# Kernel optimization log

Hardware: AMD Instinct MI355X
Metric: run time of the kernel (lower is better)

Reference implementation:

```python
import jax, jax.numpy as jnp
import numpy as np

NSIDE = 128
NPIX = 12 * NSIDE * NSIDE          # HEALPix pixel count, nested ordering
WIN = 16                           # window = 4x4 nested child block (w=1)
SHIFT = WIN // 2
EPS = 1e-5


def _ln(x, g, b):
    mu = x.mean(-1, keepdims=True)
    var = ((x - mu) ** 2).mean(-1, keepdims=True)
    return (x - mu) * jax.lax.rsqrt(var + EPS) * g + b


def _window_attn(x, wq, bq, wp, bp, n_heads):
    B, N, C = x.shape
    D = C // n_heads
    nw = N // WIN
    qkv = (x @ wq + bq).reshape(B, nw, WIN, 3, n_heads, D)
    q, k, v = jnp.moveaxis(qkv, 3, 0)
    q = jnp.swapaxes(q, 2, 3)
    k = jnp.swapaxes(k, 2, 3)
    v = jnp.swapaxes(v, 2, 3)
    scores = jnp.einsum('bwhqd,bwhkd->bwhqk', q, k) * (D ** -0.5)
    attn = jax.nn.softmax(scores, axis=-1)
    out = jnp.einsum('bwhqk,bwhkd->bwhqd', attn, v)
    out = jnp.swapaxes(out, 2, 3).reshape(B, N, C)
    return out @ wp + bp


def _transformer_block(x, p, shift, n_heads):
    if shift:
        x = jnp.roll(x, -SHIFT, axis=1)          # cyclic shift along nested index
    x = x + _window_attn(_ln(x, p['ln1_g'], p['ln1_b']),
                         p['w_qkv'], p['b_qkv'], p['w_proj'], p['b_proj'], n_heads)
    h = _ln(x, p['ln2_g'], p['ln2_b'])
    x = x + jax.nn.gelu(h @ p['w_mlp1'] + p['b_mlp1'], approximate=False) @ p['w_mlp2'] + p['b_mlp2']
    if shift:
        x = jnp.roll(x, SHIFT, axis=1)
    return x


def _forward(x, w_ff1, b_ff1, ln1_g, ln1_b, w_qkv, b_qkv, w_proj, b_proj,
             ln2_g, ln2_b, w_mlp1, b_mlp1, w_mlp2, b_mlp2, w_ff2, b_ff2,
             n_heads=4):
    residual = x
    h = jax.nn.gelu(x @ w_ff1 + b_ff1, approximate=False)
    for i, shift in enumerate((False, True)):
        p = dict(ln1_g=ln1_g[i], ln1_b=ln1_b[i], w_qkv=w_qkv[i], b_qkv=b_qkv[i],
                 w_proj=w_proj[i], b_proj=b_proj[i], ln2_g=ln2_g[i], ln2_b=ln2_b[i],
                 w_mlp1=w_mlp1[i], b_mlp1=b_mlp1[i], w_mlp2=w_mlp2[i], b_mlp2=b_mlp2[i])
        h = _transformer_block(h, p, shift, n_heads)
    return residual + h @ w_ff2 + b_ff2


def setup_inputs() -> dict:
    key = jax.random.key(0)
    ks = jax.random.split(key, 8)
    F, C, M = 64, 128, 512  # node_feat_dim, node_hidden_dim, mlp hidden
    s = 0.02
    return {
        'x': jax.random.normal(ks[0], (1, NPIX, F), jnp.float32),
        'w_ff1': jax.random.normal(ks[1], (F, C), jnp.float32) * s,
        'b_ff1': jnp.zeros((C,), jnp.float32),
        'ln1_g': jnp.ones((2, C), jnp.float32),
        'ln1_b': jnp.zeros((2, C), jnp.float32),
        'w_qkv': jax.random.normal(ks[2], (2, C, 3 * C), jnp.float32) * s,
        'b_qkv': jnp.zeros((2, 3 * C), jnp.float32),
        'w_proj': jax.random.normal(ks[3], (2, C, C), jnp.float32) * s,
        'b_proj': jnp.zeros((2, C), jnp.float32),
        'ln2_g': jnp.ones((2, C), jnp.float32),
        'ln2_b': jnp.zeros((2, C), jnp.float32),
        'w_mlp1': jax.random.normal(ks[4], (2, C, M), jnp.float32) * s,
        'b_mlp1': jnp.zeros((2, M), jnp.float32),
        'w_mlp2': jax.random.normal(ks[5], (2, M, C), jnp.float32) * s,
        'b_mlp2': jnp.zeros((2, C), jnp.float32),
        'w_ff2': jax.random.normal(ks[6], (C, F), jnp.float32) * s,
        'b_ff2': jnp.zeros((F,), jnp.float32),
    }


def reference(x, w_ff1, b_ff1, ln1_g, ln1_b, w_qkv, b_qkv, w_proj, b_proj,
              ln2_g, ln2_b, w_mlp1, b_mlp1, w_mlp2, b_mlp2, w_ff2, b_ff2):
    return _forward(x, w_ff1, b_ff1, ln1_g, ln1_b, w_qkv, b_qkv, w_proj, b_proj,
                    ln2_g, ln2_b, w_mlp1, b_mlp1, w_mlp2, b_mlp2, w_ff2, b_ff2)
```

## Files before the change

### kernel.cpp

```cpp
#include <hip/hip_runtime.h>
#include <hip/hip_bf16.h>
#include <math.h>

#define NPIX 196608
#define SCALE_Q 0.17677669529663687f

typedef __attribute__((ext_vector_type(4))) float f32x4;
typedef __attribute__((ext_vector_type(8))) short short8;
typedef __attribute__((ext_vector_type(4))) short short4v;
typedef __hip_bfloat16 bf16;

__device__ __forceinline__ float gelu_f(float x) {
    float yy = 1.5957691216057308f * (x + 0.044715f * x * x * x);
    float e = __expf(yy);
    return x - x * __builtin_amdgcn_rcpf(e + 1.0f);
}

__device__ __forceinline__ short bfbits(float f) {
    bf16 h = __float2bfloat16(f);
    return *reinterpret_cast<short*>(&h);
}

__device__ __forceinline__ short8 ldsA(const bf16* buf, int row, int el) {
    return *reinterpret_cast<const short8*>(buf + row * 128 + (el ^ ((row & 7) << 3)));
}
__device__ __forceinline__ short8 ldsA64(const bf16* buf, int row, int el) {
    return *reinterpret_cast<const short8*>(buf + row * 64 + (el ^ ((row & 7) << 3)));
}
__device__ __forceinline__ short8 gld8(const bf16* p) {
    return *reinterpret_cast<const short8*>(p);
}

__global__ __launch_bounds__(256) void k_convert(
    const float* __restrict__ wff1, const float* __restrict__ wqkv,
    const float* __restrict__ wproj, const float* __restrict__ wmlp1,
    const float* __restrict__ wmlp2, const float* __restrict__ wff2,
    bf16* __restrict__ dst)
{
    int gid = blockIdx.x * 256 + threadIdx.x;
    if (gid < 8192) {
        int n = gid >> 6, k = gid & 63;
        dst[gid] = __float2bfloat16(wff1[k * 128 + n]);
    } else if (gid < 106496) {
        int r = gid - 8192; int l = r / 49152; r -= l * 49152;
        int n = r >> 7, k = r & 127;
        dst[gid] = __float2bfloat16(wqkv[l * 49152 + k * 384 + n]);
    } else if (gid < 139264) {
        int r = gid - 106496; int l = r / 16384; r -= l * 16384;
        int n = r >> 7, k = r & 127;
        dst[gid] = __float2bfloat16(wproj[l * 16384 + k * 128 + n]);
    } else if (gid < 270336) {
        int r = gid - 139264; int l = r >> 16; r &= 65535;
        int n = r >> 7, k = r & 127;
        dst[gid] = __float2bfloat16(wmlp1[l * 65536 + k * 512 + n]);
    } else if (gid < 401408) {
        int r = gid - 270336; int l = r >> 16; r &= 65535;
        int n = r >> 9, k = r & 511;
        dst[gid] = __float2bfloat16(wmlp2[l * 65536 + k * 128 + n]);
    } else if (gid < 409600) {
        int r = gid - 401408;
        int n = r >> 7, k = r & 127;
        dst[gid] = __float2bfloat16(wff2[k * 64 + n]);
    }
}

template <int OFFSET, int MODE>
__global__ __launch_bounds__(256, 3) void k_block(
    const float* __restrict__ x, float* __restrict__ h,
    const bf16* __restrict__ wf1t, const float* __restrict__ bf1,
    const float* __restrict__ g1, const float* __restrict__ be1,
    const bf16* __restrict__ wqt, const float* __restrict__ bq,
    const bf16* __restrict__ wpt, const float* __restrict__ bp,
    const float* __restrict__ g2, const float* __restrict__ be2,
    const bf16* __restrict__ w1t, const float* __restrict__ b1,
    const bf16* __restrict__ w2t, const float* __restrict__ b2,
    const bf16* __restrict__ wf2t, const float* __restrict__ bf2,
    float* __restrict__ out)
{
    __shared__ __align__(16) bf16 bufA[8192];
    __shared__ __align__(16) bf16 bufB[8192];
    __shared__ __align__(16) bf16 bufC[8192];
    const int tid = threadIdx.x, base = blockIdx.x * 64;
    const int wid = tid >> 6, lrow = tid & 15, lgrp = (tid >> 4) & 3;
    const int cb0 = wid * 32;

    f32x4 hraw[2][4];

    if (MODE == 0) {
        short8 wf1[2][2];
#pragma unroll
        for (int nt = 0; nt < 2; ++nt)
#pragma unroll
            for (int kk = 0; kk < 2; ++kk)
                wf1[nt][kk] = gld8(wf1t + (size_t)(cb0 + nt * 16 + lrow) * 64 + kk * 32 + lgrp * 8);
        {
            int row = tid >> 2, q = tid & 3;
#pragma unroll
            for (int s = 0; s < 2; ++s) {
                int gg = q + s * 4;
                const float4* src = reinterpret_cast<const float4*>(x + (size_t)(base + row) * 64 + gg * 8);
                float4 v0 = src[0], v1 = src[1];
                short8 w;
                w[0] = bfbits(v0.x); w[1] = bfbits(v0.y); w[2] = bfbits(v0.z); w[3] = bfbits(v0.w);
                w[4] = bfbits(v1.x); w[5] = bfbits(v1.y); w[6] = bfbits(v1.z); w[7] = bfbits(v1.w);
                *reinterpret_cast<short8*>(&bufC[row * 64 + ((gg * 8) ^ ((row & 7) << 3))]) = w;
            }
        }
        __syncthreads();
        short8 xb1[4][2];
#pragma unroll
        for (int tt = 0; tt < 4; ++tt)
#pragma unroll
            for (int kk = 0; kk < 2; ++kk)
                xb1[tt][kk] = ldsA64(bufC, tt * 16 + lrow, kk * 32 + lgrp * 8);
        __syncthreads();
#pragma unroll
        for (int nt = 0; nt < 2; ++nt) {
            float4 bv = *reinterpret_cast<const float4*>(bf1 + cb0 + nt * 16 + lgrp * 4);
#pragma unroll
            for (int tt = 0; tt < 4; ++tt) {
                f32x4 d = {0.f, 0.f, 0.f, 0.f};
#pragma unroll
                for (int kk = 0; kk < 2; ++kk)
                    d = __builtin_amdgcn_mfma_f32_16x16x32_bf16(wf1[nt][kk], xb1[tt][kk], d, 0, 0, 0);
                f32x4 r;
                r[0] = gelu_f(d[0] + bv.x); r[1] = gelu_f(d[1] + bv.y);
                r[2] = gelu_f(d[2] + bv.z); r[3] = gelu_f(d[3] + bv.w);
                hraw[nt][tt] = r;
            }
        }
    } else {
#pragma unroll
        for (int nt = 0; nt < 2; ++nt)
#pragma unroll
            for (int tt = 0; tt < 4; ++tt) {
                int tok = base + OFFSET + tt * 16 + lrow; if (tok >= NPIX) tok -= NPIX;
                float4 hv = *reinterpret_cast<const float4*>(h + (size_t)tok * 128 + cb0 + nt * 16 + lgrp * 4);
                f32x4 r; r[0] = hv.x; r[1] = hv.y; r[2] = hv.z; r[3] = hv.w;
                hraw[nt][tt] = r;
            }
        __syncthreads();
    }

    float2* ws = reinterpret_cast<float2*>(bufC);
#pragma unroll
    for (int tt = 0; tt < 4; ++tt) {
        float s = 0.f, q = 0.f;
#pragma unroll
        for (int nt = 0; nt < 2; ++nt)
#pragma unroll
            for (int i = 0; i < 4; ++i) { float v = hraw[nt][tt][i]; s += v; q += v * v; }
        s += __shfl_xor(s, 16, 64); s += __shfl_xor(s, 32, 64);
        q += __shfl_xor(q, 16, 64); q += __shfl_xor(q, 32, 64);
        if (lgrp == 0) { float2 t2; t2.x = s; t2.y = q; ws[wid * 64 + tt * 16 + lrow] = t2; }
    }
    __syncthreads();
    {
        float mu[4], rstd[4];
#pragma unroll
        for (int tt = 0; tt < 4; ++tt) {
            float s = 0.f, q = 0.f;
#pragma unroll
            for (int w = 0; w < 4; ++w) {
                float2 t2 = ws[w * 64 + tt * 16 + lrow];
                s += t2.x; q += t2.y;
            }
            float m = s * (1.f / 128.f);
            mu[tt] = m;
            rstd[tt] = rsqrtf(q * (1.f / 128.f) - m * m + 1e-5f);
        }
        float4 gv[2], bev[2];
#pragma unroll
        for (int nt = 0; nt < 2; ++nt) {
            gv[nt]  = *reinterpret_cast<const float4*>(g1 + cb0 + nt * 16 + lgrp * 4);
            bev[nt] = *reinterpret_cast<const float4*>(be1 + cb0 + nt * 16 + lgrp * 4);
        }
#pragma unroll
        for (int nt = 0; nt < 2; ++nt)
#pragma unroll
            for (int tt = 0; tt < 4; ++tt) {
                short4v pk;
                pk[0] = bfbits((hraw[nt][tt][0] - mu[tt]) * rstd[tt] * gv[nt].x + bev[nt].x);
                pk[1] = bfbits((hraw[nt][tt][1] - mu[tt]) * rstd[tt] * gv[nt].y + bev[nt].y);
                pk[2] = bfbits((hraw[nt][tt][2] - mu[tt]) * rstd[tt] * gv[nt].z + bev[nt].z);
                pk[3] = bfbits((hraw[nt][tt][3] - mu[tt]) * rstd[tt] * gv[nt].w + bev[nt].w);
                int row = tt * 16 + lrow;
                int c = cb0 + nt * 16 + lgrp * 4;
                *reinterpret_cast<short4v*>(&bufA[row * 128 + (c ^ ((row & 7) << 3))]) = pk;
            }
    }

    const int qc = wid * 96;
    short8 wq0[2][4], wq1[2][4];
#pragma unroll
    for (int j = 0; j < 2; ++j)
#pragma unroll
        for (int kk = 0; kk < 4; ++kk)
            wq0[j][kk] = gld8(wqt + (size_t)(qc + j * 16 + lrow) * 128 + kk * 32 + lgrp * 8);
    __syncthreads();

    short8 xb[4][4];
#pragma unroll
    for (int tt = 0; tt < 4; ++tt)
#pragma unroll
        for (int kk = 0; kk < 4; ++kk)
            xb[tt][kk] = ldsA(bufA, tt * 16 + lrow, kk * 32 + lgrp * 8);
    __syncthreads();

#define QKV_TILE(WF, NB)                                                            \
    {                                                                               \
        const int cb = qc + (NB) * 16;                                              \
        float4 bqv = *reinterpret_cast<const float4*>(bq + cb + lgrp * 4);          \
        _Pragma("unroll")                                                           \
        for (int tt = 0; tt < 4; ++tt) {                                            \
            f32x4 d = {0.f, 0.f, 0.f, 0.f};                                         \
            _Pragma("unroll")                                                       \
            for (int kk = 0; kk < 4; ++kk)                                          \
                d = __builtin_amdgcn_mfma_f32_16x16x32_bf16(WF[kk], xb[tt][kk], d, 0, 0, 0); \
            int row = tt * 16 + lrow;                                               \
            if (cb < 128) {                                                         \
                int c = cb + lgrp * 4;                                              \
                short4v pk;                                                         \
                pk[0] = bfbits((d[0] + bqv.x) * SCALE_Q); pk[1] = bfbits((d[1] + bqv.y) * SCALE_Q); \
                pk[2] = bfbits((d[2] + bqv.z) * SCALE_Q); pk[3] = bfbits((d[3] + bqv.w) * SCALE_Q); \
                *reinterpret_cast<short4v*>(&bufA[row * 128 + (c ^ ((row & 7) << 3))]) = pk; \
            } else if (cb < 256) {                                                  \
                int c = cb - 128 + lgrp * 4;                                        \
                short4v pk;                                                         \
                pk[0] = bfbits(d[0] + bqv.x); pk[1] = bfbits(d[1] + bqv.y);         \
                pk[2] = bfbits(d[2] + bqv.z); pk[3] = bfbits(d[3] + bqv.w);         \
                *reinterpret_cast<short4v*>(&bufB[row * 128 + (c ^ ((row & 7) << 3))]) = pk; \
            } else {                                                                \
                int db = cb - 256 + lgrp * 4;                                       \
                bufC[tt * 2048 + (db + 0) * 16 + lrow] = __float2bfloat16(d[0] + bqv.x); \
                bufC[tt * 2048 + (db + 1) * 16 + lrow] = __float2bfloat16(d[1] + bqv.y); \
                bufC[tt * 2048 + (db + 2) * 16 + lrow] = __float2bfloat16(d[2] + bqv.z); \
                bufC[tt * 2048 + (db + 3) * 16 + lrow] = __float2bfloat16(d[3] + bqv.w); \
            }                                                                       \
        }                                                                           \
    }

#pragma unroll
    for (int j = 0; j < 2; ++j)
#pragma unroll
        for (int kk = 0; kk < 4; ++kk)
            wq1[j][kk] = gld8(wqt + (size_t)(qc + (j + 2) * 16 + lrow) * 128 + kk * 32 + lgrp * 8);
    QKV_TILE(wq0[0], 0) QKV_TILE(wq0[1], 1)
#pragma unroll
    for (int j = 0; j < 2; ++j)
#pragma unroll
        for (int kk = 0; kk < 4; ++kk)
            wq0[j][kk] = gld8(wqt + (size_t)(qc + (j + 4) * 16 + lrow) * 128 + kk * 32 + lgrp * 8);
    QKV_TILE(wq1[0], 2) QKV_TILE(wq1[1], 3)
    QKV_TILE(wq0[0], 4) QKV_TILE(wq0[1], 5)
    __syncthreads();

    short8 wfp[2][4];
#pragma unroll
    for (int nt = 0; nt < 2; ++nt)
#pragma unroll
        for (int kk = 0; kk < 4; ++kk)
            wfp[nt][kk] = gld8(wpt + (size_t)(cb0 + nt * 16 + lrow) * 128 + kk * 32 + lgrp * 8);

    float p[4][4];
#pragma unroll
    for (int hh = 0; hh < 4; ++hh) {
        short8 aq = ldsA(bufA, wid * 16 + lrow, hh * 32 + lgrp * 8);
        short8 bk = ldsA(bufB, wid * 16 + lrow, hh * 32 + lgrp * 8);
        f32x4 z = {0.f, 0.f, 0.f, 0.f};
        f32x4 s = __builtin_amdgcn_mfma_f32_16x16x32_bf16(aq, bk, z, 0, 0, 0);
#pragma unroll
        for (int i = 0; i < 4; ++i) {
            float m_ = s[i];
            m_ = fmaxf(m_, __shfl_xor(m_, 1, 64));
            m_ = fmaxf(m_, __shfl_xor(m_, 2, 64));
            m_ = fmaxf(m_, __shfl_xor(m_, 4, 64));
            m_ = fmaxf(m_, __shfl_xor(m_, 8, 64));
            float e = __expf(s[i] - m_);
            float sum = e;
            sum += __shfl_xor(sum, 1, 64);
            sum += __shfl_xor(sum, 2, 64);
            sum += __shfl_xor(sum, 4, 64);
            sum += __shfl_xor(sum, 8, 64);
            p[hh][i] = e * __builtin_amdgcn_rcpf(sum);
        }
    }
    bf16* pl = bufB + wid * 2048;
#pragma unroll
    for (int hh = 0; hh < 4; ++hh)
#pragma unroll
        for (int i = 0; i < 4; ++i)
            pl[hh * 256 + (lgrp * 4 + i) * 16 + lrow] = __float2bfloat16(p[hh][i]);

    short8 z8 = {0, 0, 0, 0, 0, 0, 0, 0};
#pragma unroll
    for (int dt = 0; dt < 8; ++dt) {
        int hh = dt >> 1;
        short8 av = z8, bv = z8;
        if (lgrp < 2) {
            av = *reinterpret_cast<const short8*>(&bufC[wid * 2048 + (dt * 16 + lrow) * 16 + lgrp * 8]);
            bv = *reinterpret_cast<const short8*>(&pl[hh * 256 + lrow * 16 + lgrp * 8]);
        }
        f32x4 z = {0.f, 0.f, 0.f, 0.f};
        f32x4 o = __builtin_amdgcn_mfma_f32_16x16x32_bf16(av, bv, z, 0, 0, 0);
        int row = wid * 16 + lrow;
        int c = dt * 16 + lgrp * 4;
        short4v pk;
        pk[0] = bfbits(o[0]); pk[1] = bfbits(o[1]); pk[2] = bfbits(o[2]); pk[3] = bfbits(o[3]);
        *reinterpret_cast<short4v*>(&bufA[row * 128 + (c ^ ((row & 7) << 3))]) = pk;
    }
    __syncthreads();

    short8 af[4][4];
#pragma unroll
    for (int tt = 0; tt < 4; ++tt)
#pragma unroll
        for (int kk = 0; kk < 4; ++kk)
            af[tt][kk] = ldsA(bufA, tt * 16 + lrow, kk * 32 + lgrp * 8);
    f32x4 hres[2][4];
#pragma unroll
    for (int nt = 0; nt < 2; ++nt) {
        float4 bpv = *reinterpret_cast<const float4*>(bp + cb0 + nt * 16 + lgrp * 4);
#pragma unroll
        for (int tt = 0; tt < 4; ++tt) {
            f32x4 d = {0.f, 0.f, 0.f, 0.f};
#pragma unroll
            for (int kk = 0; kk < 4; ++kk)
                d = __builtin_amdgcn_mfma_f32_16x16x32_bf16(wfp[nt][kk], af[tt][kk], d, 0, 0, 0);
            f32x4 r = hraw[nt][tt];
            r[0] += bpv.x + d[0]; r[1] += bpv.y + d[1];
            r[2] += bpv.z + d[2]; r[3] += bpv.w + d[3];
            hres[nt][tt] = r;
        }
    }

#pragma unroll
    for (int tt = 0; tt < 4; ++tt) {
        float s = 0.f, q = 0.f;
#pragma unroll
        for (int nt = 0; nt < 2; ++nt)
#pragma unroll
            for (int i = 0; i < 4; ++i) { float v = hres[nt][tt][i]; s += v; q += v * v; }
        s += __shfl_xor(s, 16, 64); s += __shfl_xor(s, 32, 64);
        q += __shfl_xor(q, 16, 64); q += __shfl_xor(q, 32, 64);
        if (lgrp == 0) { float2 t2; t2.x = s; t2.y = q; ws[wid * 64 + tt * 16 + lrow] = t2; }
    }
    __syncthreads();
    short8 w1f[2][2][4];
    {
        float mu[4], rstd[4];
#pragma unroll
        for (int tt = 0; tt < 4; ++tt) {
            float s = 0.f, q = 0.f;
#pragma unroll
            for (int w = 0; w < 4; ++w) {
                float2 t2 = ws[w * 64 + tt * 16 + lrow];
                s += t2.x; q += t2.y;
            }
            float m = s * (1.f / 128.f);
            mu[tt] = m;
            rstd[tt] = rsqrtf(q * (1.f / 128.f) - m * m + 1e-5f);
        }
        float4 gv[2], bev[2];
#pragma unroll
        for (int nt = 0; nt < 2; ++nt) {
            gv[nt]  = *reinterpret_cast<const float4*>(g2 + cb0 + nt * 16 + lgrp * 4);
            bev[nt] = *reinterpret_cast<const float4*>(be2 + cb0 + nt * 16 + lgrp * 4);
        }
#pragma unroll
        for (int nt = 0; nt < 2; ++nt)
#pragma unroll
            for (int tt = 0; tt < 4; ++tt) {
                short4v pk;
                pk[0] = bfbits((hres[nt][tt][0] - mu[tt]) * rstd[tt] * gv[nt].x + bev[nt].x);
                pk[1] = bfbits((hres[nt][tt][1] - mu[tt]) * rstd[tt] * gv[nt].y + bev[nt].y);
                pk[2] = bfbits((hres[nt][tt][2] - mu[tt]) * rstd[tt] * gv[nt].z + bev[nt].z);
                pk[3] = bfbits((hres[nt][tt][3] - mu[tt]) * rstd[tt] * gv[nt].w + bev[nt].w);
                int row = tt * 16 + lrow;
                int c = cb0 + nt * 16 + lgrp * 4;
                *reinterpret_cast<short4v*>(&bufB[row * 128 + (c ^ ((row & 7) << 3))]) = pk;
            }
    }
#pragma unroll
    for (int nt = 0; nt < 2; ++nt)
#pragma unroll
        for (int kk = 0; kk < 4; ++kk)
            w1f[0][nt][kk] = gld8(w1t + (size_t)(cb0 + nt * 16 + lrow) * 128 + kk * 32 + lgrp * 8);
    __syncthreads();

    f32x4 acc2[2][4];
#pragma unroll
    for (int nt = 0; nt < 2; ++nt)
#pragma unroll
        for (int tt = 0; tt < 4; ++tt) acc2[nt][tt] = (f32x4){0.f, 0.f, 0.f, 0.f};

#pragma unroll
    for (int ch = 0; ch < 4; ++ch) {
        short8 w2f[2][4];
#pragma unroll
        for (int nt = 0; nt < 2; ++nt)
#pragma unroll
            for (int kk = 0; kk < 4; ++kk)
                w2f[nt][kk] = gld8(w2t + (size_t)(cb0 + nt * 16 + lrow) * 512 + ch * 128 + kk * 32 + lgrp * 8);
        float4 b1v[2];
#pragma unroll
        for (int nt = 0; nt < 2; ++nt)
            b1v[nt] = *reinterpret_cast<const float4*>(b1 + ch * 128 + cb0 + nt * 16 + lgrp * 4);
#pragma unroll
        for (int tt = 0; tt < 4; ++tt) {
            short8 xf[4];
#pragma unroll
            for (int kk = 0; kk < 4; ++kk)
                xf[kk] = ldsA(bufB, tt * 16 + lrow, kk * 32 + lgrp * 8);
#pragma unroll
            for (int nt = 0; nt < 2; ++nt) {
                f32x4 d = {0.f, 0.f, 0.f, 0.f};
#pragma unroll
                for (int kk = 0; kk < 4; ++kk)
                    d = __builtin_amdgcn_mfma_f32_16x16x32_bf16(w1f[ch & 1][nt][kk], xf[kk], d, 0, 0, 0);
                short4v pk;
                pk[0] = bfbits(gelu_f(d[0] + b1v[nt].x)); pk[1] = bfbits(gelu_f(d[1] + b1v[nt].y));
                pk[2] = bfbits(gelu_f(d[2] + b1v[nt].z)); pk[3] = bfbits(gelu_f(d[3] + b1v[nt].w));
                int row = tt * 16 + lrow;
                int c = cb0 + nt * 16 + lgrp * 4;
                *reinterpret_cast<short4v*>(&bufA[row * 128 + (c ^ ((row & 7) << 3))]) = pk;
            }
        }
        __syncthreads();
        if (ch < 3) {
#pragma unroll
            for (int nt = 0; nt < 2; ++nt)
#pragma unroll
                for (int kk = 0; kk < 4; ++kk)
                    w1f[(ch + 1) & 1][nt][kk] =
                        gld8(w1t + (size_t)((ch + 1) * 128 + cb0 + nt * 16 + lrow) * 128 + kk * 32 + lgrp * 8);
        }
#pragma unroll
        for (int tt = 0; tt < 4; ++tt) {
            short8 uf[4];
#pragma unroll
            for (int kk = 0; kk < 4; ++kk)
                uf[kk] = ldsA(bufA, tt * 16 + lrow, kk * 32 + lgrp * 8);
#pragma unroll
            for (int nt = 0; nt < 2; ++nt)
#pragma unroll
                for (int kk = 0; kk < 4; ++kk)
                    acc2[nt][tt] = __builtin_amdgcn_mfma_f32_16x16x32_bf16(
                        w2f[nt][kk], uf[kk], acc2[nt][tt], 0, 0, 0);
        }
        __syncthreads();
    }

    if (MODE == 0) {
#pragma unroll
        for (int nt = 0; nt < 2; ++nt) {
            const int n0 = cb0 + nt * 16 + lgrp * 4;
            float4 b2v = *reinterpret_cast<const float4*>(b2 + n0);
#pragma unroll
            for (int tt = 0; tt < 4; ++tt) {
                int tok = base + OFFSET + tt * 16 + lrow; if (tok >= NPIX) tok -= NPIX;
                float4 ov;
                ov.x = hres[nt][tt][0] + b2v.x + acc2[nt][tt][0];
                ov.y = hres[nt][tt][1] + b2v.y + acc2[nt][tt][1];
                ov.z = hres[nt][tt][2] + b2v.z + acc2[nt][tt][2];
                ov.w = hres[nt][tt][3] + b2v.w + acc2[nt][tt][3];
                *reinterpret_cast<float4*>(h + (size_t)tok * 128 + n0) = ov;
            }
        }
    } else {
        short8 wff[4];
#pragma unroll
        for (int kk = 0; kk < 4; ++kk)
            wff[kk] = gld8(wf2t + (size_t)(wid * 16 + lrow) * 128 + kk * 32 + lgrp * 8);
        float4 xv[4];
#pragma unroll
        for (int tt = 0; tt < 4; ++tt) {
            int tok = base + OFFSET + tt * 16 + lrow; if (tok >= NPIX) tok -= NPIX;
            xv[tt] = *reinterpret_cast<const float4*>(x + (size_t)tok * 64 + wid * 16 + lgrp * 4);
        }
#pragma unroll
        for (int nt = 0; nt < 2; ++nt) {
            const int n0 = cb0 + nt * 16 + lgrp * 4;
            float4 b2v = *reinterpret_cast<const float4*>(b2 + n0);
#pragma unroll
            for (int tt = 0; tt < 4; ++tt) {
                short4v pk;
                pk[0] = bfbits(hres[nt][tt][0] + b2v.x + acc2[nt][tt][0]);
                pk[1] = bfbits(hres[nt][tt][1] + b2v.y + acc2[nt][tt][1]);
                pk[2] = bfbits(hres[nt][tt][2] + b2v.z + acc2[nt][tt][2]);
                pk[3] = bfbits(hres[nt][tt][3] + b2v.w + acc2[nt][tt][3]);
                int row = tt * 16 + lrow;
                int c = cb0 + nt * 16 + lgrp * 4;
                *reinterpret_cast<short4v*>(&bufB[row * 128 + (c ^ ((row & 7) << 3))]) = pk;
            }
        }
        __syncthreads();
        float4 bfv = *reinterpret_cast<const float4*>(bf2 + wid * 16 + lgrp * 4);
#pragma unroll
        for (int tt = 0; tt < 4; ++tt) {
            short8 bfr[4];
#pragma unroll
            for (int kk = 0; kk < 4; ++kk)
                bfr[kk] = ldsA(bufB, tt * 16 + lrow, kk * 32 + lgrp * 8);
            f32x4 d = {0.f, 0.f, 0.f, 0.f};
#pragma unroll
            for (int kk = 0; kk < 4; ++kk)
                d = __builtin_amdgcn_mfma_f32_16x16x32_bf16(wff[kk], bfr[kk], d, 0, 0, 0);
            int tok = base + OFFSET + tt * 16 + lrow; if (tok >= NPIX) tok -= NPIX;
            float4 ov;
            ov.x = xv[tt].x + bfv.x + d[0]; ov.y = xv[tt].y + bfv.y + d[1];
            ov.z = xv[tt].z + bfv.z + d[2]; ov.w = xv[tt].w + bfv.w + d[3];
            *reinterpret_cast<float4*>(out + (size_t)tok * 64 + wid * 16 + lgrp * 4) = ov;
        }
    }
#undef QKV_TILE
}

extern "C" void kernel_launch(void* const* d_in, const int* in_sizes, int n_in,
                              void* d_out, int out_size, void* d_ws, size_t ws_size,
                              hipStream_t stream) {
    (void)in_sizes; (void)n_in; (void)out_size; (void)ws_size;
    const float* x      = (const float*)d_in[0];
    const float* w_ff1  = (const float*)d_in[1];
    const float* b_ff1  = (const float*)d_in[2];
    const float* ln1_g  = (const float*)d_in[3];
    const float* ln1_b  = (const float*)d_in[4];
    const float* w_qkv  = (const float*)d_in[5];
    const float* b_qkv  = (const float*)d_in[6];
    const float* w_proj = (const float*)d_in[7];
    const float* b_proj = (const float*)d_in[8];
    const float* ln2_g  = (const float*)d_in[9];
    const float* ln2_b  = (const float*)d_in[10];
    const float* w_mlp1 = (const float*)d_in[11];
    const float* b_mlp1 = (const float*)d_in[12];
    const float* w_mlp2 = (const float*)d_in[13];
    const float* b_mlp2 = (const float*)d_in[14];
    const float* w_ff2  = (const float*)d_in[15];
    const float* b_ff2  = (const float*)d_in[16];
    float* out = (float*)d_out;

    float* h = (float*)d_ws;
    bf16* wbf = (bf16*)((char*)d_ws + (size_t)NPIX * 128 * 4);
    bf16* ff1t  = wbf;
    bf16* qkvt  = wbf + 8192;
    bf16* projt = wbf + 106496;
    bf16* mlp1t = wbf + 139264;
    bf16* mlp2t = wbf + 270336;
    bf16* ff2t  = wbf + 401408;

    dim3 blk(256);
    k_convert<<<1600, blk, 0, stream>>>(w_ff1, w_qkv, w_proj, w_mlp1, w_mlp2, w_ff2, wbf);

    const int NB = NPIX / 64;
    k_block<0, 0><<<NB, blk, 0, stream>>>(x, h,
        ff1t, b_ff1,
        ln1_g, ln1_b, qkvt, b_qkv, projt, b_proj,
        ln2_g, ln2_b, mlp1t, b_mlp1, mlp2t, b_mlp2,
        ff2t, b_ff2, out);

    k_block<8, 1><<<NB, blk, 0, stream>>>(x, h,
        ff1t, b_ff1,
        ln1_g + 128, ln1_b + 128, qkvt + 49152, b_qkv + 384, projt + 16384, b_proj + 128,
        ln2_g + 128, ln2_b + 128, mlp1t + 65536, b_mlp1 + 512, mlp2t + 65536, b_mlp2 + 128,
        ff2t, b_ff2, out);
}
```

Baseline: 488.0 us.

## Restructure block kernel to one wavefront per 16-token window without barriers

Each workgroup now holds a single 64-lane wavefront that owns one 16-token window and computes all 128 output channels itself. The old design had 256 threads handling 64 tokens with channels split across four waves. Because one wave now does everything, the __syncthreads barriers and the cross-wave LayerNorm reduction through shared memory disappear, and LDS per block shrinks to 16 KB. In exchange, every wave streams the full weight matrices from global/L2 memory, with no sharing across waves and no prefetch double-buffering, so weight traffic per token rises roughly fourfold. It also uses 4x more blocks.

```diff
diff --git a/kernel.cpp b/kernel.cpp
--- a/kernel.cpp
+++ b/kernel.cpp
@@ -21,12 +21,6 @@
     return *reinterpret_cast<short*>(&h);
 }
 
-__device__ __forceinline__ short8 ldsA(const bf16* buf, int row, int el) {
-    return *reinterpret_cast<const short8*>(buf + row * 128 + (el ^ ((row & 7) << 3)));
-}
-__device__ __forceinline__ short8 ldsA64(const bf16* buf, int row, int el) {
-    return *reinterpret_cast<const short8*>(buf + row * 64 + (el ^ ((row & 7) << 3)));
-}
 __device__ __forceinline__ short8 gld8(const bf16* p) {
     return *reinterpret_cast<const short8*>(p);
 }
@@ -65,7 +59,7 @@
 }
 
 template <int OFFSET, int MODE>
-__global__ __launch_bounds__(256, 3) void k_block(
+__global__ __launch_bounds__(64, 2) void k_block(
     const float* __restrict__ x, float* __restrict__ h,
     const bf16* __restrict__ wf1t, const float* __restrict__ bf1,
     const float* __restrict__ g1, const float* __restrict__ be1,
@@ -77,196 +71,139 @@
     const bf16* __restrict__ wf2t, const float* __restrict__ bf2,
     float* __restrict__ out)
 {
-    __shared__ __align__(16) bf16 bufA[8192];
-    __shared__ __align__(16) bf16 bufB[8192];
-    __shared__ __align__(16) bf16 bufC[8192];
-    const int tid = threadIdx.x, base = blockIdx.x * 64;
-    const int wid = tid >> 6, lrow = tid & 15, lgrp = (tid >> 4) & 3;
-    const int cb0 = wid * 32;
-
-    f32x4 hraw[2][4];
+    __shared__ __align__(16) bf16 S[8192];
+    bf16* XN1 = S;
+    bf16* QQ  = S + 2048;
+    bf16* KK  = S + 4096;
+    bf16* VT  = S + 6144;
+    const int lane = threadIdx.x;
+    const int lrow = lane & 15, lgrp = lane >> 4;
+    const int base = blockIdx.x * 16;
+    int tok = base + OFFSET + lrow; if (tok >= NPIX) tok -= NPIX;
+    const int sw = (lrow & 7) << 3;
+
+    f32x4 hraw[8];
 
     if (MODE == 0) {
-        short8 wf1[2][2];
-#pragma unroll
-        for (int nt = 0; nt < 2; ++nt)
+        const float4* src = reinterpret_cast<const float4*>(x + (size_t)(base + lrow) * 64 + lgrp * 16);
+        float4 v0 = src[0], v1 = src[1], v2 = src[2], v3 = src[3];
+        short8 w0, w1;
+        w0[0]=bfbits(v0.x); w0[1]=bfbits(v0.y); w0[2]=bfbits(v0.z); w0[3]=bfbits(v0.w);
+        w0[4]=bfbits(v1.x); w0[5]=bfbits(v1.y); w0[6]=bfbits(v1.z); w0[7]=bfbits(v1.w);
+        w1[0]=bfbits(v2.x); w1[1]=bfbits(v2.y); w1[2]=bfbits(v2.z); w1[3]=bfbits(v2.w);
+        w1[4]=bfbits(v3.x); w1[5]=bfbits(v3.y); w1[6]=bfbits(v3.z); w1[7]=bfbits(v3.w);
+        *reinterpret_cast<short8*>(&KK[lrow * 64 + ((lgrp * 16) ^ sw)]) = w0;
+        *reinterpret_cast<short8*>(&KK[lrow * 64 + ((lgrp * 16 + 8) ^ sw)]) = w1;
+        short8 xb1[2];
+#pragma unroll
+        for (int kk = 0; kk < 2; ++kk)
+            xb1[kk] = *reinterpret_cast<const short8*>(&KK[lrow * 64 + ((kk * 32 + lgrp * 8) ^ sw)]);
+#pragma unroll
+        for (int nt = 0; nt < 8; ++nt) {
+            short8 wf[2];
 #pragma unroll
             for (int kk = 0; kk < 2; ++kk)
-                wf1[nt][kk] = gld8(wf1t + (size_t)(cb0 + nt * 16 + lrow) * 64 + kk * 32 + lgrp * 8);
-        {
-            int row = tid >> 2, q = tid & 3;
-#pragma unroll
-            for (int s = 0; s < 2; ++s) {
-                int gg = q + s * 4;
-                const float4* src = reinterpret_cast<const float4*>(x + (size_t)(base + row) * 64 + gg * 8);
-                float4 v0 = src[0], v1 = src[1];
-                short8 w;
-                w[0] = bfbits(v0.x); w[1] = bfbits(v0.y); w[2] = bfbits(v0.z); w[3] = bfbits(v0.w);
-                w[4] = bfbits(v1.x); w[5] = bfbits(v1.y); w[6] = bfbits(v1.z); w[7] = bfbits(v1.w);
-                *reinterpret_cast<short8*>(&bufC[row * 64 + ((gg * 8) ^ ((row & 7) << 3))]) = w;
-            }
-        }
-        __syncthreads();
-        short8 xb1[4][2];
-#pragma unroll
-        for (int tt = 0; tt < 4; ++tt)
+                wf[kk] = gld8(wf1t + (size_t)(nt * 16 + lrow) * 64 + kk * 32 + lgrp * 8);
+            f32x4 d = {0.f, 0.f, 0.f, 0.f};
 #pragma unroll
             for (int kk = 0; kk < 2; ++kk)
-                xb1[tt][kk] = ldsA64(bufC, tt * 16 + lrow, kk * 32 + lgrp * 8);
-        __syncthreads();
-#pragma unroll
-        for (int nt = 0; nt < 2; ++nt) {
-            float4 bv = *reinterpret_cast<const float4*>(bf1 + cb0 + nt * 16 + lgrp * 4);
-#pragma unroll
-            for (int tt = 0; tt < 4; ++tt) {
-                f32x4 d = {0.f, 0.f, 0.f, 0.f};
-#pragma unroll
-                for (int kk = 0; kk < 2; ++kk)
-                    d = __builtin_amdgcn_mfma_f32_16x16x32_bf16(wf1[nt][kk], xb1[tt][kk], d, 0, 0, 0);
-                f32x4 r;
-                r[0] = gelu_f(d[0] + bv.x); r[1] = gelu_f(d[1] + bv.y);
-                r[2] = gelu_f(d[2] + bv.z); r[3] = gelu_f(d[3] + bv.w);
-                hraw[nt][tt] = r;
-            }
+                d = __builtin_amdgcn_mfma_f32_16x16x32_bf16(wf[kk], xb1[kk], d, 0, 0, 0);
+            float4 bv = *reinterpret_cast<const float4*>(bf1 + nt * 16 + lgrp * 4);
+            f32x4 r;
+            r[0] = gelu_f(d[0] + bv.x); r[1] = gelu_f(d[1] + bv.y);
+            r[2] = gelu_f(d[2] + bv.z); r[3] = gelu_f(d[3] + bv.w);
+            hraw[nt] = r;
         }
     } else {
 #pragma unroll
-        for (int nt = 0; nt < 2; ++nt)
-#pragma unroll
-            for (int tt = 0; tt < 4; ++tt) {
-                int tok = base + OFFSET + tt * 16 + lrow; if (tok >= NPIX) tok -= NPIX;
-                float4 hv = *reinterpret_cast<const float4*>(h + (size_t)tok * 128 + cb0 + nt * 16 + lgrp * 4);
-                f32x4 r; r[0] = hv.x; r[1] = hv.y; r[2] = hv.z; r[3] = hv.w;
-                hraw[nt][tt] = r;
-            }
-        __syncthreads();
-    }
-
-    float2* ws = reinterpret_cast<float2*>(bufC);
-#pragma unroll
-    for (int tt = 0; tt < 4; ++tt) {
+        for (int nt = 0; nt < 8; ++nt) {
+            float4 hv = *reinterpret_cast<const float4*>(h + (size_t)tok * 128 + nt * 16 + lgrp * 4);
+            f32x4 r; r[0] = hv.x; r[1] = hv.y; r[2] = hv.z; r[3] = hv.w;
+            hraw[nt] = r;
+        }
+    }
+
+    {
         float s = 0.f, q = 0.f;
 #pragma unroll
-        for (int nt = 0; nt < 2; ++nt)
-#pragma unroll
-            for (int i = 0; i < 4; ++i) { float v = hraw[nt][tt][i]; s += v; q += v * v; }
+        for (int nt = 0; nt < 8; ++nt)
+#pragma unroll
+            for (int i = 0; i < 4; ++i) { float v = hraw[nt][i]; s += v; q += v * v; }
         s += __shfl_xor(s, 16, 64); s += __shfl_xor(s, 32, 64);
         q += __shfl_xor(q, 16, 64); q += __shfl_xor(q, 32, 64);
-        if (lgrp == 0) { float2 t2; t2.x = s; t2.y = q; ws[wid * 64 + tt * 16 + lrow] = t2; }
-    }
-    __syncthreads();
-    {
-        float mu[4], rstd[4];
-#pragma unroll
-        for (int tt = 0; tt < 4; ++tt) {
-            float s = 0.f, q = 0.f;
-#pragma unroll
-            for (int w = 0; w < 4; ++w) {
-                float2 t2 = ws[w * 64 + tt * 16 + lrow];
-                s += t2.x; q += t2.y;
-            }
-            float m = s * (1.f / 128.f);
-            mu[tt] = m;
-            rstd[tt] = rsqrtf(q * (1.f / 128.f) - m * m + 1e-5f);
-        }
-        float4 gv[2], bev[2];
-#pragma unroll
-        for (int nt = 0; nt < 2; ++nt) {
-            gv[nt]  = *reinterpret_cast<const float4*>(g1 + cb0 + nt * 16 + lgrp * 4);
-            bev[nt] = *reinterpret_cast<const float4*>(be1 + cb0 + nt * 16 + lgrp * 4);
-        }
-#pragma unroll
-        for (int nt = 0; nt < 2; ++nt)
-#pragma unroll
-            for (int tt = 0; tt < 4; ++tt) {
-                short4v pk;
-                pk[0] = bfbits((hraw[nt][tt][0] - mu[tt]) * rstd[tt] * gv[nt].x + bev[nt].x);
-                pk[1] = bfbits((hraw[nt][tt][1] - mu[tt]) * rstd[tt] * gv[nt].y + bev[nt].y);
-                pk[2] = bfbits((hraw[nt][tt][2] - mu[tt]) * rstd[tt] * gv[nt].z + bev[nt].z);
-                pk[3] = bfbits((hraw[nt][tt][3] - mu[tt]) * rstd[tt] * gv[nt].w + bev[nt].w);
-                int row = tt * 16 + lrow;
-                int c = cb0 + nt * 16 + lgrp * 4;
-                *reinterpret_cast<short4v*>(&bufA[row * 128 + (c ^ ((row & 7) << 3))]) = pk;
-            }
-    }
-
-    const int qc = wid * 96;
-    short8 wq0[2][4], wq1[2][4];
-#pragma unroll
-    for (int j = 0; j < 2; ++j)
-#pragma unroll
-        for (int kk = 0; kk < 4; ++kk)
-            wq0[j][kk] = gld8(wqt + (size_t)(qc + j * 16 + lrow) * 128 + kk * 32 + lgrp * 8);
-    __syncthreads();
-
-    short8 xb[4][4];
-#pragma unroll
-    for (int tt = 0; tt < 4; ++tt)
-#pragma unroll
-        for (int kk = 0; kk < 4; ++kk)
-            xb[tt][kk] = ldsA(bufA, tt * 16 + lrow, kk * 32 + lgrp * 8);
-    __syncthreads();
-
-#define QKV_TILE(WF, NB)                                                            \
-    {                                                                               \
-        const int cb = qc + (NB) * 16;                                              \
-        float4 bqv = *reinterpret_cast<const float4*>(bq + cb + lgrp * 4);          \
-        _Pragma("unroll")                                                           \
-        for (int tt = 0; tt < 4; ++tt) {                                            \
-            f32x4 d = {0.f, 0.f, 0.f, 0.f};                                         \
-            _Pragma("unroll")                                                       \
-            for (int kk = 0; kk < 4; ++kk)                                          \
-                d = __builtin_amdgcn_mfma_f32_16x16x32_bf16(WF[kk], xb[tt][kk], d, 0, 0, 0); \
-            int row = tt * 16 + lrow;                                               \
-            if (cb < 128) {                                                         \
-                int c = cb + lgrp * 4;                                              \
-                short4v pk;                                                         \
-                pk[0] = bfbits((d[0] + bqv.x) * SCALE_Q); pk[1] = bfbits((d[1] + bqv.y) * SCALE_Q); \
-                pk[2] = bfbits((d[2] + bqv.z) * SCALE_Q); pk[3] = bfbits((d[3] + bqv.w) * SCALE_Q); \
-                *reinterpret_cast<short4v*>(&bufA[row * 128 + (c ^ ((row & 7) << 3))]) = pk; \
-            } else if (cb < 256) {                                                  \
-                int c = cb - 128 + lgrp * 4;                                        \
-                short4v pk;                                                         \
-                pk[0] = bfbits(d[0] + bqv.x); pk[1] = bfbits(d[1] + bqv.y);         \
-                pk[2] = bfbits(d[2] + bqv.z); pk[3] = bfbits(d[3] + bqv.w);         \
-                *reinterpret_cast<short4v*>(&bufB[row * 128 + (c ^ ((row & 7) << 3))]) = pk; \
-            } else {                                                                \
-                int db = cb - 256 + lgrp * 4;                                       \
-                bufC[tt * 2048 + (db + 0) * 16 + lrow] = __float2bfloat16(d[0] + bqv.x); \
-                bufC[tt * 2048 + (db + 1) * 16 + lrow] = __float2bfloat16(d[1] + bqv.y); \
-                bufC[tt * 2048 + (db + 2) * 16 + lrow] = __float2bfloat16(d[2] + bqv.z); \
-                bufC[tt * 2048 + (db + 3) * 16 + lrow] = __float2bfloat16(d[3] + bqv.w); \
-            }                                                                       \
-        }                                                                           \
-    }
-
-#pragma unroll
-    for (int j = 0; j < 2; ++j)
-#pragma unroll
-        for (int kk = 0; kk < 4; ++kk)
-            wq1[j][kk] = gld8(wqt + (size_t)(qc + (j + 2) * 16 + lrow) * 128 + kk * 32 + lgrp * 8);
-    QKV_TILE(wq0[0], 0) QKV_TILE(wq0[1], 1)
-#pragma unroll
-    for (int j = 0; j < 2; ++j)
-#pragma unroll
-        for (int kk = 0; kk < 4; ++kk)
-            wq0[j][kk] = gld8(wqt + (size_t)(qc + (j + 4) * 16 + lrow) * 128 + kk * 32 + lgrp * 8);
-    QKV_TILE(wq1[0], 2) QKV_TILE(wq1[1], 3)
-    QKV_TILE(wq0[0], 4) QKV_TILE(wq0[1], 5)
-    __syncthreads();
-
-    short8 wfp[2][4];
-#pragma unroll
-    for (int nt = 0; nt < 2; ++nt)
-#pragma unroll
-        for (int kk = 0; kk < 4; ++kk)
-            wfp[nt][kk] = gld8(wpt + (size_t)(cb0 + nt * 16 + lrow) * 128 + kk * 32 + lgrp * 8);
+        float mu = s * (1.f / 128.f);
+        float rstd = rsqrtf(q * (1.f / 128.f) - mu * mu + 1e-5f);
+#pragma unroll
+        for (int nt = 0; nt < 8; ++nt) {
+            float4 gv  = *reinterpret_cast<const float4*>(g1 + nt * 16 + lgrp * 4);
+            float4 bev = *reinterpret_cast<const float4*>(be1 + nt * 16 + lgrp * 4);
+            short4v pk;
+            pk[0] = bfbits((hraw[nt][0] - mu) * rstd * gv.x + bev.x);
+            pk[1] = bfbits((hraw[nt][1] - mu) * rstd * gv.y + bev.y);
+            pk[2] = bfbits((hraw[nt][2] - mu) * rstd * gv.z + bev.z);
+            pk[3] = bfbits((hraw[nt][3] - mu) * rstd * gv.w + bev.w);
+            *reinterpret_cast<short4v*>(&XN1[lrow * 128 + ((nt * 16 + lgrp * 4) ^ sw)]) = pk;
+        }
+    }
+    short8 xb[4];
+#pragma unroll
+    for (int kk = 0; kk < 4; ++kk)
+        xb[kk] = *reinterpret_cast<const short8*>(&XN1[lrow * 128 + ((kk * 32 + lgrp * 8) ^ sw)]);
+
+#pragma unroll
+    for (int nt = 0; nt < 8; ++nt) {
+        short8 wf[4];
+#pragma unroll
+        for (int kk = 0; kk < 4; ++kk)
+            wf[kk] = gld8(wqt + (size_t)(nt * 16 + lrow) * 128 + kk * 32 + lgrp * 8);
+        f32x4 d = {0.f, 0.f, 0.f, 0.f};
+#pragma unroll
+        for (int kk = 0; kk < 4; ++kk)
+            d = __builtin_amdgcn_mfma_f32_16x16x32_bf16(wf[kk], xb[kk], d, 0, 0, 0);
+        float4 bv = *reinterpret_cast<const float4*>(bq + nt * 16 + lgrp * 4);
+        short4v pk;
+        pk[0] = bfbits((d[0] + bv.x) * SCALE_Q); pk[1] = bfbits((d[1] + bv.y) * SCALE_Q);
+        pk[2] = bfbits((d[2] + bv.z) * SCALE_Q); pk[3] = bfbits((d[3] + bv.w) * SCALE_Q);
+        *reinterpret_cast<short4v*>(&QQ[lrow * 128 + ((nt * 16 + lgrp * 4) ^ sw)]) = pk;
+    }
+#pragma unroll
+    for (int nt = 0; nt < 8; ++nt) {
+        short8 wf[4];
+#pragma unroll
+        for (int kk = 0; kk < 4; ++kk)
+            wf[kk] = gld8(wqt + (size_t)(128 + nt * 16 + lrow) * 128 + kk * 32 + lgrp * 8);
+        f32x4 d = {0.f, 0.f, 0.f, 0.f};
+#pragma unroll
+        for (int kk = 0; kk < 4; ++kk)
+            d = __builtin_amdgcn_mfma_f32_16x16x32_bf16(wf[kk], xb[kk], d, 0, 0, 0);
+        float4 bv = *reinterpret_cast<const float4*>(bq + 128 + nt * 16 + lgrp * 4);
+        short4v pk;
+        pk[0] = bfbits(d[0] + bv.x); pk[1] = bfbits(d[1] + bv.y);
+        pk[2] = bfbits(d[2] + bv.z); pk[3] = bfbits(d[3] + bv.w);
+        *reinterpret_cast<short4v*>(&KK[lrow * 128 + ((nt * 16 + lgrp * 4) ^ sw)]) = pk;
+    }
+#pragma unroll
+    for (int dt = 0; dt < 8; ++dt) {
+        short8 wv[4];
+#pragma unroll
+        for (int kk = 0; kk < 4; ++kk)
+            wv[kk] = gld8(wqt + (size_t)(256 + dt * 16 + lrow) * 128 + kk * 32 + lgrp * 8);
+        f32x4 d = {0.f, 0.f, 0.f, 0.f};
+#pragma unroll
+        for (int kk = 0; kk < 4; ++kk)
+            d = __builtin_amdgcn_mfma_f32_16x16x32_bf16(xb[kk], wv[kk], d, 0, 0, 0);
+        float bv = bq[256 + dt * 16 + lrow];
+        short4v pk;
+        pk[0] = bfbits(d[0] + bv); pk[1] = bfbits(d[1] + bv);
+        pk[2] = bfbits(d[2] + bv); pk[3] = bfbits(d[3] + bv);
+        *reinterpret_cast<short4v*>(&VT[(dt * 16 + lrow) * 16 + lgrp * 4]) = pk;
+    }
 
     float p[4][4];
 #pragma unroll
     for (int hh = 0; hh < 4; ++hh) {
-        short8 aq = ldsA(bufA, wid * 16 + lrow, hh * 32 + lgrp * 8);
-        short8 bk = ldsA(bufB, wid * 16 + lrow, hh * 32 + lgrp * 8);
+        short8 aq = *reinterpret_cast<const short8*>(&QQ[lrow * 128 + ((hh * 32 + lgrp * 8) ^ sw)]);
+        short8 bk = *reinterpret_cast<const short8*>(&KK[lrow * 128 + ((hh * 32 + lgrp * 8) ^ sw)]);
         f32x4 z = {0.f, 0.f, 0.f, 0.f};
         f32x4 s = __builtin_amdgcn_mfma_f32_16x16x32_bf16(aq, bk, z, 0, 0, 0);
 #pragma unroll
@@ -285,12 +222,11 @@
             p[hh][i] = e * __builtin_amdgcn_rcpf(sum);
         }
     }
-    bf16* pl = bufB + wid * 2048;
 #pragma unroll
     for (int hh = 0; hh < 4; ++hh)
 #pragma unroll
         for (int i = 0; i < 4; ++i)
-            pl[hh * 256 + (lgrp * 4 + i) * 16 + lrow] = __float2bfloat16(p[hh][i]);
+            QQ[hh * 256 + (lgrp * 4 + i) * 16 + lrow] = __float2bfloat16(p[hh][i]);
 
     short8 z8 = {0, 0, 0, 0, 0, 0, 0, 0};
 #pragma unroll
@@ -298,222 +234,148 @@
         int hh = dt >> 1;
         short8 av = z8, bv = z8;
         if (lgrp < 2) {
-            av = *reinterpret_cast<const short8*>(&bufC[wid * 2048 + (dt * 16 + lrow) * 16 + lgrp * 8]);
-            bv = *reinterpret_cast<const short8*>(&pl[hh * 256 + lrow * 16 + lgrp * 8]);
+            av = *reinterpret_cast<const short8*>(&VT[(dt * 16 + lrow) * 16 + lgrp * 8]);
+            bv = *reinterpret_cast<const short8*>(&QQ[hh * 256 + lrow * 16 + lgrp * 8]);
         }
         f32x4 z = {0.f, 0.f, 0.f, 0.f};
         f32x4 o = __builtin_amdgcn_mfma_f32_16x16x32_bf16(av, bv, z, 0, 0, 0);
-        int row = wid * 16 + lrow;
-        int c = dt * 16 + lgrp * 4;
         short4v pk;
         pk[0] = bfbits(o[0]); pk[1] = bfbits(o[1]); pk[2] = bfbits(o[2]); pk[3] = bfbits(o[3]);
-        *reinterpret_cast<short4v*>(&bufA[row * 128 + (c ^ ((row & 7) << 3))]) = pk;
-    }
-    __syncthreads();
-
-    short8 af[4][4];
-#pragma unroll
-    for (int tt = 0; tt < 4; ++tt)
-#pragma unroll
-        for (int kk = 0; kk < 4; ++kk)
-            af[tt][kk] = ldsA(bufA, tt * 16 + lrow, kk * 32 + lgrp * 8);
-    f32x4 hres[2][4];
-#pragma unroll
-    for (int nt = 0; nt < 2; ++nt) {
-        float4 bpv = *reinterpret_cast<const float4*>(bp + cb0 + nt * 16 + lgrp * 4);
-#pragma unroll
-        for (int tt = 0; tt < 4; ++tt) {
-            f32x4 d = {0.f, 0.f, 0.f, 0.f};
-#pragma unroll
-            for (int kk = 0; kk < 4; ++kk)
-                d = __builtin_amdgcn_mfma_f32_16x16x32_bf16(wfp[nt][kk], af[tt][kk], d, 0, 0, 0);
-            f32x4 r = hraw[nt][tt];
-            r[0] += bpv.x + d[0]; r[1] += bpv.y + d[1];
-            r[2] += bpv.z + d[2]; r[3] += bpv.w + d[3];
-            hres[nt][tt] = r;
-        }
-    }
-
-#pragma unroll
-    for (int tt = 0; tt < 4; ++tt) {
+        *reinterpret_cast<short4v*>(&XN1[lrow * 128 + ((dt * 16 + lgrp * 4) ^ sw)]) = pk;
+    }
+
+    short8 af[4];
+#pragma unroll
+    for (int kk = 0; kk < 4; ++kk)
+        af[kk] = *reinterpret_cast<const short8*>(&XN1[lrow * 128 + ((kk * 32 + lgrp * 8) ^ sw)]);
+    f32x4 hres[8];
+#pragma unroll
+    for (int nt = 0; nt < 8; ++nt) {
+        short8 wf[4];
+#pragma unroll
+        for (int kk = 0; kk < 4; ++kk)
+            wf[kk] = gld8(wpt + (size_t)(nt * 16 + lrow) * 128 + kk * 32 + lgrp * 8);
+        f32x4 d = {0.f, 0.f, 0.f, 0.f};
+#pragma unroll
+        for (int kk = 0; kk < 4; ++kk)
+            d = __builtin_amdgcn_mfma_f32_16x16x32_bf16(wf[kk], af[kk], d, 0, 0, 0);
+        float4 bv = *reinterpret_cast<const float4*>(bp + nt * 16 + lgrp * 4);
+        f32x4 r = hraw[nt];
+        r[0] += bv.x + d[0]; r[1] += bv.y + d[1];
+        r[2] += bv.z + d[2]; r[3] += bv.w + d[3];
+        hres[nt] = r;
+    }
+
+    {
         float s = 0.f, q = 0.f;
 #pragma unroll
-        for (int nt = 0; nt < 2; ++nt)
-#pragma unroll
-            for (int i = 0; i < 4; ++i) { float v = hres[nt][tt][i]; s += v; q += v * v; }
+        for (int nt = 0; nt < 8; ++nt)
+#pragma unroll
+            for (int i = 0; i < 4; ++i) { float v = hres[nt][i]; s += v; q += v * v; }
         s += __shfl_xor(s, 16, 64); s += __shfl_xor(s, 32, 64);
         q += __shfl_xor(q, 16, 64); q += __shfl_xor(q, 32, 64);
-        if (lgrp == 0) { float2 t2; t2.x = s; t2.y = q; ws[wid * 64 + tt * 16 + lrow] = t2; }
-    }
-    __syncthreads();
-    short8 w1f[2][2][4];
-    {
-        float mu[4], rstd[4];
-#pragma unroll
-        for (int tt = 0; tt < 4; ++tt) {
-            float s = 0.f, q = 0.f;
-#pragma unroll
-            for (int w = 0; w < 4; ++w) {
-                float2 t2 = ws[w * 64 + tt * 16 + lrow];
-                s += t2.x; q += t2.y;
-            }
-            float m = s * (1.f / 128.f);
-            mu[tt] = m;
-            rstd[tt] = rsqrtf(q * (1.f / 128.f) - m * m + 1e-5f);
-        }
-        float4 gv[2], bev[2];
-#pragma unroll
-        for (int nt = 0; nt < 2; ++nt) {
-            gv[nt]  = *reinterpret_cast<const float4*>(g2 + cb0 + nt * 16 + lgrp * 4);
-            bev[nt] = *reinterpret_cast<const float4*>(be2 + cb0 + nt * 16 + lgrp * 4);
-        }
-#pragma unroll
-        for (int nt = 0; nt < 2; ++nt)
-#pragma unroll
-            for (int tt = 0; tt < 4; ++tt) {
-                short4v pk;
-                pk[0] = bfbits((hres[nt][tt][0] - mu[tt]) * rstd[tt] * gv[nt].x + bev[nt].x);
-                pk[1] = bfbits((hres[nt][tt][1] - mu[tt]) * rstd[tt] * gv[nt].y + bev[nt].y);
-                pk[2] = bfbits((hres[nt][tt][2] - mu[tt]) * rstd[tt] * gv[nt].z + bev[nt].z);
-                pk[3] = bfbits((hres[nt][tt][3] - mu[tt]) * rstd[tt] * gv[nt].w + bev[nt].w);
-                int row = tt * 16 + lrow;
-                int c = cb0 + nt * 16 + lgrp * 4;
-                *reinterpret_cast<short4v*>(&bufB[row * 128 + (c ^ ((row & 7) << 3))]) = pk;
-            }
-    }
-#pragma unroll
-    for (int nt = 0; nt < 2; ++nt)
-#pragma unroll
-        for (int kk = 0; kk < 4; ++kk)
-            w1f[0][nt][kk] = gld8(w1t + (size_t)(cb0 + nt * 16 + lrow) * 128 + kk * 32 + lgrp * 8);
-    __syncthreads();
-
-    f32x4 acc2[2][4];
-#pragma unroll
-    for (int nt = 0; nt < 2; ++nt)
-#pragma unroll
-        for (int tt = 0; tt < 4; ++tt) acc2[nt][tt] = (f32x4){0.f, 0.f, 0.f, 0.f};
-
+        float mu = s * (1.f / 128.f);
+        float rstd = rsqrtf(q * (1.f / 128.f) - mu * mu + 1e-5f);
+#pragma unroll
+        for (int nt = 0; nt < 8; ++nt) {
+            float4 gv  = *reinterpret_cast<const float4*>(g2 + nt * 16 + lgrp * 4);
+            float4 bev = *reinterpret_cast<const float4*>(be2 + nt * 16 + lgrp * 4);
+            short4v pk;
+            pk[0] = bfbits((hres[nt][0] - mu) * rstd * gv.x + bev.x);
+            pk[1] = bfbits((hres[nt][1] - mu) * rstd * gv.y + bev.y);
+            pk[2] = bfbits((hres[nt][2] - mu) * rstd * gv.z + bev.z);
+            pk[3] = bfbits((hres[nt][3] - mu) * rstd * gv.w + bev.w);
+            *reinterpret_cast<short4v*>(&QQ[lrow * 128 + ((nt * 16 + lgrp * 4) ^ sw)]) = pk;
+        }
+    }
+    short8 xb2[4];
+#pragma unroll
+    for (int kk = 0; kk < 4; ++kk)
+        xb2[kk] = *reinterpret_cast<const short8*>(&QQ[lrow * 128 + ((kk * 32 + lgrp * 8) ^ sw)]);
+
+    f32x4 acc2[8];
+#pragma unroll
+    for (int nt = 0; nt < 8; ++nt) acc2[nt] = (f32x4){0.f, 0.f, 0.f, 0.f};
 #pragma unroll
     for (int ch = 0; ch < 4; ++ch) {
-        short8 w2f[2][4];
-#pragma unroll
-        for (int nt = 0; nt < 2; ++nt)
-#pragma unroll
-            for (int kk = 0; kk < 4; ++kk)
-                w2f[nt][kk] = gld8(w2t + (size_t)(cb0 + nt * 16 + lrow) * 512 + ch * 128 + kk * 32 + lgrp * 8);
-        float4 b1v[2];
-#pragma unroll
-        for (int nt = 0; nt < 2; ++nt)
-            b1v[nt] = *reinterpret_cast<const float4*>(b1 + ch * 128 + cb0 + nt * 16 + lgrp * 4);
-#pragma unroll
-        for (int tt = 0; tt < 4; ++tt) {
-            short8 xf[4];
-#pragma unroll
-            for (int kk = 0; kk < 4; ++kk)
-                xf[kk] = ldsA(bufB, tt * 16 + lrow, kk * 32 + lgrp * 8);
-#pragma unroll
-            for (int nt = 0; nt < 2; ++nt) {
-                f32x4 d = {0.f, 0.f, 0.f, 0.f};
-#pragma unroll
-                for (int kk = 0; kk < 4; ++kk)
-                    d = __builtin_amdgcn_mfma_f32_16x16x32_bf16(w1f[ch & 1][nt][kk], xf[kk], d, 0, 0, 0);
-                short4v pk;
-                pk[0] = bfbits(gelu_f(d[0] + b1v[nt].x)); pk[1] = bfbits(gelu_f(d[1] + b1v[nt].y));
-                pk[2] = bfbits(gelu_f(d[2] + b1v[nt].z)); pk[3] = bfbits(gelu_f(d[3] + b1v[nt].w));
-                int row = tt * 16 + lrow;
-                int c = cb0 + nt * 16 + lgrp * 4;
-                *reinterpret_cast<short4v*>(&bufA[row * 128 + (c ^ ((row & 7) << 3))]) = pk;
-            }
-        }
-        __syncthreads();
-        if (ch < 3) {
-#pragma unroll
-            for (int nt = 0; nt < 2; ++nt)
-#pragma unroll
-                for (int kk = 0; kk < 4; ++kk)
-                    w1f[(ch + 1) & 1][nt][kk] =
-                        gld8(w1t + (size_t)((ch + 1) * 128 + cb0 + nt * 16 + lrow) * 128 + kk * 32 + lgrp * 8);
-        }
-#pragma unroll
-        for (int tt = 0; tt < 4; ++tt) {
-            short8 uf[4];
-#pragma unroll
-            for (int kk = 0; kk < 4; ++kk)
-                uf[kk] = ldsA(bufA, tt * 16 + lrow, kk * 32 + lgrp * 8);
-#pragma unroll
-            for (int nt = 0; nt < 2; ++nt)
-#pragma unroll
-                for (int kk = 0; kk < 4; ++kk)
-                    acc2[nt][tt] = __builtin_amdgcn_mfma_f32_16x16x32_bf16(
-                        w2f[nt][kk], uf[kk], acc2[nt][tt], 0, 0, 0);
-        }
-        __syncthreads();
+        bf16* UB = (ch & 1) ? VT : KK;
+#pragma unroll
+        for (int nt = 0; nt < 8; ++nt) {
+            short8 wf[4];
+#pragma unroll
+            for (int kk = 0; kk < 4; ++kk)
+                wf[kk] = gld8(w1t + (size_t)(ch * 128 + nt * 16 + lrow) * 128 + kk * 32 + lgrp * 8);
+            f32x4 d = {0.f, 0.f, 0.f, 0.f};
+#pragma unroll
+            for (int kk = 0; kk < 4; ++kk)
+                d = __builtin_amdgcn_mfma_f32_16x16x32_bf16(wf[kk], xb2[kk], d, 0, 0, 0);
+            float4 bv = *reinterpret_cast<const float4*>(b1 + ch * 128 + nt * 16 + lgrp * 4);
+            short4v pk;
+            pk[0] = bfbits(gelu_f(d[0] + bv.x)); pk[1] = bfbits(gelu_f(d[1] + bv.y));
+            pk[2] = bfbits(gelu_f(d[2] + bv.z)); pk[3] = bfbits(gelu_f(d[3] + bv.w));
+            *reinterpret_cast<short4v*>(&UB[lrow * 128 + ((nt * 16 + lgrp * 4) ^ sw)]) = pk;
+        }
+        short8 uf[4];
+#pragma unroll
+        for (int kk = 0; kk < 4; ++kk)
+            uf[kk] = *reinterpret_cast<const short8*>(&UB[lrow * 128 + ((kk * 32 + lgrp * 8) ^ sw)]);
+#pragma unroll
+        for (int nt = 0; nt < 8; ++nt) {
+            short8 wf[4];
+#pragma unroll
+            for (int kk = 0; kk < 4; ++kk)
+                wf[kk] = gld8(w2t + (size_t)(nt * 16 + lrow) * 512 + ch * 128 + kk * 32 + lgrp * 8);
+#pragma unroll
+            for (int kk = 0; kk < 4; ++kk)
+                acc2[nt] = __builtin_amdgcn_mfma_f32_16x16x32_bf16(wf[kk], uf[kk], acc2[nt], 0, 0, 0);
+        }
     }
 
     if (MODE == 0) {
 #pragma unroll
-        for (int nt = 0; nt < 2; ++nt) {
-            const int n0 = cb0 + nt * 16 + lgrp * 4;
-            float4 b2v = *reinterpret_cast<const float4*>(b2 + n0);
-#pragma unroll
-            for (int tt = 0; tt < 4; ++tt) {
-                int tok = base + OFFSET + tt * 16 + lrow; if (tok >= NPIX) tok -= NPIX;
-                float4 ov;
-                ov.x = hres[nt][tt][0] + b2v.x + acc2[nt][tt][0];
-                ov.y = hres[nt][tt][1] + b2v.y + acc2[nt][tt][1];
-                ov.z = hres[nt][tt][2] + b2v.z + acc2[nt][tt][2];
-                ov.w = hres[nt][tt][3] + b2v.w + acc2[nt][tt][3];
-                *reinterpret_cast<float4*>(h + (size_t)tok * 128 + n0) = ov;
-            }
+        for (int nt = 0; nt < 8; ++nt) {
+            float4 b2v = *reinterpret_cast<const float4*>(b2 + nt * 16 + lgrp * 4);
+            float4 ov;
+            ov.x = hres[nt][0] + b2v.x + acc2[nt][0];
+            ov.y = hres[nt][1] + b2v.y + acc2[nt][1];
+            ov.z = hres[nt][2] + b2v.z + acc2[nt][2];
+            ov.w = hres[nt][3] + b2v.w + acc2[nt][3];
+            *reinterpret_cast<float4*>(h + (size_t)tok * 128 + nt * 16 + lgrp * 4) = ov;
         }
     } else {
-        short8 wff[4];
-#pragma unroll
-        for (int kk = 0; kk < 4; ++kk)
-            wff[kk] = gld8(wf2t + (size_t)(wid * 16 + lrow) * 128 + kk * 32 + lgrp * 8);
-        float4 xv[4];
-#pragma unroll
-        for (int tt = 0; tt < 4; ++tt) {
-            int tok = base + OFFSET + tt * 16 + lrow; if (tok >= NPIX) tok -= NPIX;
-            xv[tt] = *reinterpret_cast<const float4*>(x + (size_t)tok * 64 + wid * 16 + lgrp * 4);
-        }
-#pragma unroll
-        for (int nt = 0; nt < 2; ++nt) {
-            const int n0 = cb0 + nt * 16 + lgrp * 4;
-            float4 b2v = *reinterpret_cast<const float4*>(b2 + n0);
-#pragma unroll
-            for (int tt = 0; tt < 4; ++tt) {
-                short4v pk;
-                pk[0] = bfbits(hres[nt][tt][0] + b2v.x + acc2[nt][tt][0]);
-                pk[1] = bfbits(hres[nt][tt][1] + b2v.y + acc2[nt][tt][1]);
-                pk[2] = bfbits(hres[nt][tt][2] + b2v.z + acc2[nt][tt][2]);
-                pk[3] = bfbits(hres[nt][tt][3] + b2v.w + acc2[nt][tt][3]);
-                int row = tt * 16 + lrow;
-                int c = cb0 + nt * 16 + lgrp * 4;
-                *reinterpret_cast<short4v*>(&bufB[row * 128 + (c ^ ((row & 7) << 3))]) = pk;
-            }
-        }
-        __syncthreads();
-        float4 bfv = *reinterpret_cast<const float4*>(bf2 + wid * 16 + lgrp * 4);
-#pragma unroll
-        for (int tt = 0; tt < 4; ++tt) {
-            short8 bfr[4];
-#pragma unroll
-            for (int kk = 0; kk < 4; ++kk)
-                bfr[kk] = ldsA(bufB, tt * 16 + lrow, kk * 32 + lgrp * 8);
+#pragma unroll
+        for (int nt = 0; nt < 8; ++nt) {
+            float4 b2v = *reinterpret_cast<const float4*>(b2 + nt * 16 + lgrp * 4);
+            short4v pk;
+            pk[0] = bfbits(hres[nt][0] + b2v.x + acc2[nt][0]);
+            pk[1] = bfbits(hres[nt][1] + b2v.y + acc2[nt][1]);
+            pk[2] = bfbits(hres[nt][2] + b2v.z + acc2[nt][2]);
+            pk[3] = bfbits(hres[nt][3] + b2v.w + acc2[nt][3]);
+            *reinterpret_cast<short4v*>(&KK[lrow * 128 + ((nt * 16 + lgrp * 4) ^ sw)]) = pk;
+        }
+        short8 bfr[4];
+#pragma unroll
+        for (int kk = 0; kk < 4; ++kk)
+            bfr[kk] = *reinterpret_cast<const short8*>(&KK[lrow * 128 + ((kk * 32 + lgrp * 8) ^ sw)]);
+#pragma unroll
+        for (int nt = 0; nt < 4; ++nt) {
+            short8 wf[4];
+#pragma unroll
+            for (int kk = 0; kk < 4; ++kk)
+                wf[kk] = gld8(wf2t + (size_t)(nt * 16 + lrow) * 128 + kk * 32 + lgrp * 8);
             f32x4 d = {0.f, 0.f, 0.f, 0.f};
 #pragma unroll
             for (int kk = 0; kk < 4; ++kk)
-                d = __builtin_amdgcn_mfma_f32_16x16x32_bf16(wff[kk], bfr[kk], d, 0, 0, 0);
-            int tok = base + OFFSET + tt * 16 + lrow; if (tok >= NPIX) tok -= NPIX;
+                d = __builtin_amdgcn_mfma_f32_16x16x32_bf16(wf[kk], bfr[kk], d, 0, 0, 0);
+            float4 bv = *reinterpret_cast<const float4*>(bf2 + nt * 16 + lgrp * 4);
+            size_t gidx = (size_t)tok * 64 + nt * 16 + lgrp * 4;
+            float4 xv = *reinterpret_cast<const float4*>(x + gidx);
             float4 ov;
-            ov.x = xv[tt].x + bfv.x + d[0]; ov.y = xv[tt].y + bfv.y + d[1];
-            ov.z = xv[tt].z + bfv.z + d[2]; ov.w = xv[tt].w + bfv.w + d[3];
-            *reinterpret_cast<float4*>(out + (size_t)tok * 64 + wid * 16 + lgrp * 4) = ov;
-        }
-    }
-#undef QKV_TILE
+            ov.x = xv.x + bv.x + d[0]; ov.y = xv.y + bv.y + d[1];
+            ov.z = xv.z + bv.z + d[2]; ov.w = xv.w + bv.w + d[3];
+            *reinterpret_cast<float4*>(out + gidx) = ov;
+        }
+    }
 }
 
 extern "C" void kernel_launch(void* const* d_in, const int* in_sizes, int n_in,
@@ -548,17 +410,16 @@
     bf16* mlp2t = wbf + 270336;
     bf16* ff2t  = wbf + 401408;
 
-    dim3 blk(256);
-    k_convert<<<1600, blk, 0, stream>>>(w_ff1, w_qkv, w_proj, w_mlp1, w_mlp2, w_ff2, wbf);
-
-    const int NB = NPIX / 64;
-    k_block<0, 0><<<NB, blk, 0, stream>>>(x, h,
+    k_convert<<<1600, dim3(256), 0, stream>>>(w_ff1, w_qkv, w_proj, w_mlp1, w_mlp2, w_ff2, wbf);
+
+    const int NB = NPIX / 16;
+    k_block<0, 0><<<NB, dim3(64), 0, stream>>>(x, h,
         ff1t, b_ff1,
         ln1_g, ln1_b, qkvt, b_qkv, projt, b_proj,
         ln2_g, ln2_b, mlp1t, b_mlp1, mlp2t, b_mlp2,
         ff2t, b_ff2, out);
 
-    k_block<8, 1><<<NB, blk, 0, stream>>>(x, h,
+    k_block<8, 1><<<NB, dim3(64), 0, stream>>>(x, h,
         ff1t, b_ff1,
         ln1_g + 128, ln1_b + 128, qkvt + 49152, b_qkv + 384, projt + 16384, b_proj + 128,
         ln2_g + 128, ln2_b + 128, mlp1t + 65536, b_mlp1 + 512, mlp2t + 65536, b_mlp2 + 128,
```

Result: slower. 1.149 ms (+135.4%).
